# Kernel tuning notes

Hardware: AMD Instinct MI355X
Metric: run time of the kernel (lower is better)

## Reference

```python
import jax, jax.numpy as jnp
import numpy as np

D_MODEL = 1024
HEADS = 16
DK = D_MODEL // HEADS
LAYERS = 4
BATCH = 8
SEQ = 1024
EPS = 1e-5


def _ln2(x):
    # torch LayerNorm([seq_len, d_model]) with default (untrained) affine: gamma=1, beta=0
    m = jnp.mean(x, axis=(1, 2), keepdims=True)
    v = jnp.var(x, axis=(1, 2), keepdims=True)
    return (x - m) * jax.lax.rsqrt(v + EPS)


def _pos_enc(seq_len, d_model):
    pos = jnp.arange(seq_len, dtype=jnp.float32)[:, None]
    i = jnp.arange(d_model)
    angle = pos / jnp.power(1000.0, (2 * (i // 2)).astype(jnp.float32) / d_model)
    return jnp.where(i % 2 == 0, jnp.sin(angle), jnp.cos(angle))  # [S, D]


def setup_inputs() -> dict:
    key = jax.random.key(0)
    ks = jax.random.split(key, 12)
    s = 0.02
    X = jax.random.normal(ks[0], (BATCH, SEQ, D_MODEL), dtype=jnp.float32)
    Wq = jax.random.normal(ks[1], (LAYERS, HEADS, DK, D_MODEL), dtype=jnp.float32) * s
    Wk = jax.random.normal(ks[2], (LAYERS, HEADS, DK, D_MODEL), dtype=jnp.float32) * s
    Wv = jax.random.normal(ks[3], (LAYERS, HEADS, DK, D_MODEL), dtype=jnp.float32) * s
    W0 = jax.random.normal(ks[4], (LAYERS, D_MODEL, D_MODEL), dtype=jnp.float32) * s
    Wr_w = jax.random.normal(ks[5], (LAYERS, D_MODEL, D_MODEL), dtype=jnp.float32) * s
    Wr_b = jax.random.normal(ks[6], (LAYERS, D_MODEL), dtype=jnp.float32) * s
    Wf0_w = jax.random.normal(ks[7], (LAYERS, D_MODEL, D_MODEL), dtype=jnp.float32) * s
    Wf0_b = jax.random.normal(ks[8], (LAYERS, D_MODEL), dtype=jnp.float32) * s
    Wf1_w = jax.random.normal(ks[9], (LAYERS, D_MODEL, D_MODEL), dtype=jnp.float32) * s
    Wf1_b = jax.random.normal(ks[10], (LAYERS, D_MODEL), dtype=jnp.float32) * s
    return {"X": X, "Wq": Wq, "Wk": Wk, "Wv": Wv, "W0": W0,
            "Wr_w": Wr_w, "Wr_b": Wr_b, "Wf0_w": Wf0_w, "Wf0_b": Wf0_b,
            "Wf1_w": Wf1_w, "Wf1_b": Wf1_b}


def reference(X, Wq, Wk, Wv, W0, Wr_w, Wr_b, Wf0_w, Wf0_b, Wf1_w, Wf1_b):
    B, S, D = X.shape
    x = X + _pos_enc(S, D)[None]
    scale = 1.0 / jnp.sqrt(jnp.float32(DK))
    for l in range(LAYERS):
        # batched multi-head projections (equivalent to per-head Linear + concat)
        Q = jnp.einsum('bsd,hkd->bhsk', x, Wq[l])
        K = jnp.einsum('bsd,hkd->bhsk', x, Wk[l])
        V = jnp.einsum('bsd,hkd->bhsk', x, Wv[l])
        scores = jnp.einsum('bhsk,bhtk->bhst', Q, K) * scale
        A = jax.nn.softmax(scores, axis=-1)
        O = jnp.einsum('bhst,bhtk->bhsk', A, V)
        O = O.transpose(0, 2, 1, 3).reshape(B, S, D)  # concat heads on feature dim
        mha = O @ W0[l].T
        r0 = _ln2(x + mha) @ Wr_w[l].T + Wr_b[l]
        ff = jax.nn.relu(r0 @ Wf0_w[l].T + Wf0_b[l]) @ Wf1_w[l].T + Wf1_b[l]
        x = _ln2(ff + r0) @ Wr_w[l].T + Wr_b[l]
    return x
```

## Files before the change

kernel.cpp:

```cpp
#include <hip/hip_runtime.h>
#include <hip/hip_bf16.h>
#include <math.h>

#define D_MODEL 1024
#define HEADS   16
#define DKV     64
#define LAYERS  4
#define BATCH   8
#define SEQ     1024
#define NTOK    (BATCH*SEQ)
#define LN_N    (SEQ*D_MODEL)
#define EPSV    1e-5f

typedef __attribute__((ext_vector_type(8))) short short8;
typedef __attribute__((ext_vector_type(4))) float floatx4;

__device__ __forceinline__ float bf2f(ushort u) {
    union { uint i; float f; } v; v.i = ((uint)u) << 16; return v.f;
}
__device__ __forceinline__ ushort f2bf(float f) {
    union { float f; uint i; } v; v.f = f;
    uint r = (v.i + 0x7fffu + ((v.i >> 16) & 1u)) >> 16;
    return (ushort)r;
}
__device__ __forceinline__ uint cvtpk(float a, float b) {
    uint r;
    asm("v_cvt_pk_bf16_f32 %0, %1, %2" : "=v"(r) : "v"(a), "v"(b));
    return r;
}

__device__ __forceinline__ void gload16(const ushort* g, ushort* l) {
    __builtin_amdgcn_global_load_lds(
        (const __attribute__((address_space(1))) void*)g,
        (__attribute__((address_space(3))) void*)l, 16, 0, 0);
}

__device__ __forceinline__ void gemm_core128(
    const ushort* __restrict__ A, const ushort* __restrict__ B,
    int lda, int ldb, int Kd,
    ushort* ldsA, ushort* ldsB, floatx4 (&acc)[4][4])
{
    const int tid  = threadIdx.x;
    const int lane = tid & 63;
    const int w    = tid >> 6;
    const int wm   = w >> 1, wn = w & 1;
    const int mn   = lane & 15, quad = lane >> 4;
    const int srow = tid >> 2;
    const int scol = (tid & 3) * 8;
    const ushort* ga = A + (size_t)srow * lda + scol;
    const ushort* gb = B + (size_t)srow * ldb + scol;
    ushort* la = ldsA + srow * 32 + scol;
    ushort* lb = ldsB + srow * 32 + scol;

    for (int k0 = 0; k0 < Kd; k0 += 32) {
        gload16(ga + k0, la);
        gload16(ga + (size_t)64 * lda + k0, la + 64 * 32);
        gload16(gb + k0, lb);
        gload16(gb + (size_t)64 * ldb + k0, lb + 64 * 32);
        __syncthreads();
        short8 af[4], bfr[4];
#pragma unroll
        for (int i = 0; i < 4; i++)
            af[i] = *(const short8*)(ldsA + (wm * 64 + i * 16 + mn) * 32 + quad * 8);
#pragma unroll
        for (int j = 0; j < 4; j++)
            bfr[j] = *(const short8*)(ldsB + (wn * 64 + j * 16 + mn) * 32 + quad * 8);
#pragma unroll
        for (int i = 0; i < 4; i++)
#pragma unroll
            for (int j = 0; j < 4; j++)
                acc[i][j] = __builtin_amdgcn_mfma_f32_16x16x32_bf16(af[i], bfr[j], acc[i][j], 0, 0, 0);
        __syncthreads();
    }
}

__global__ __launch_bounds__(256) void gemm_bt128(
    const ushort* __restrict__ A, const ushort* __restrict__ B,
    const float* __restrict__ bias, ushort* __restrict__ C,
    const ushort* __restrict__ resid, float* __restrict__ stats,
    float* __restrict__ outF, int relu)
{
    __shared__ ushort ldsA[128 * 32], ldsB[128 * 32];
    __shared__ float sred1[4], sred2[4];
    floatx4 acc[4][4];
#pragma unroll
    for (int i = 0; i < 4; i++)
#pragma unroll
        for (int j = 0; j < 4; j++) acc[i][j] = (floatx4){0.f, 0.f, 0.f, 0.f};

    gemm_core128(A + (size_t)blockIdx.x * 128 * D_MODEL,
                 B + (size_t)blockIdx.y * 128 * D_MODEL,
                 D_MODEL, D_MODEL, D_MODEL, ldsA, ldsB, acc);

    const int lane = threadIdx.x & 63, w = threadIdx.x >> 6;
    const int wm = w >> 1, wn = w & 1;
    const int mn = lane & 15, quad = lane >> 4;
    float ssum = 0.f, ssq = 0.f;
#pragma unroll
    for (int i = 0; i < 4; i++) {
#pragma unroll
        for (int j = 0; j < 4; j++) {
            int col = blockIdx.y * 128 + wn * 64 + j * 16 + mn;
            float bv = bias ? bias[col] : 0.f;
#pragma unroll
            for (int r = 0; r < 4; r++) {
                int row = blockIdx.x * 128 + wm * 64 + i * 16 + quad * 4 + r;
                float v = acc[i][j][r] + bv;
                if (relu) v = fmaxf(v, 0.f);
                if (resid) {
                    v += bf2f(resid[(size_t)row * D_MODEL + col]);
                    ssum += v; ssq += v * v;
                }
                if (outF) outF[(size_t)row * D_MODEL + col] = v;
                else      C[(size_t)row * D_MODEL + col] = f2bf(v);
            }
        }
    }
    if (stats) {
        for (int o = 1; o < 64; o <<= 1) {
            ssum += __shfl_xor(ssum, o); ssq += __shfl_xor(ssq, o);
        }
        if (lane == 0) { sred1[w] = ssum; sred2[w] = ssq; }
        __syncthreads();
        if (threadIdx.x == 0) {
            int b = blockIdx.x >> 3;
            atomicAdd(&stats[b * 32],      sred1[0] + sred1[1] + sred1[2] + sred1[3]);
            atomicAdd(&stats[b * 32 + 16], sred2[0] + sred2[1] + sred2[2] + sred2[3]);
        }
    }
}

__global__ __launch_bounds__(256) void gemm_qkv(
    const ushort* __restrict__ X, const ushort* __restrict__ Wq,
    const ushort* __restrict__ Wk, const ushort* __restrict__ Wv,
    ushort* __restrict__ Q, ushort* __restrict__ K, ushort* __restrict__ Vt)
{
    __shared__ ushort ldsA[128 * 32], ldsB[128 * 32];
    const int which = blockIdx.y >> 3;
    const int nb = blockIdx.y & 7;
    const ushort* B = (which == 0) ? Wq : (which == 1) ? Wk : Wv;
    floatx4 acc[4][4];
#pragma unroll
    for (int i = 0; i < 4; i++)
#pragma unroll
        for (int j = 0; j < 4; j++) acc[i][j] = (floatx4){0.f, 0.f, 0.f, 0.f};

    gemm_core128(X + (size_t)blockIdx.x * 128 * D_MODEL,
                 B + (size_t)nb * 128 * D_MODEL,
                 D_MODEL, D_MODEL, D_MODEL, ldsA, ldsB, acc);

    const int lane = threadIdx.x & 63, w = threadIdx.x >> 6;
    const int wm = w >> 1, wn = w & 1;
    const int mn = lane & 15, quad = lane >> 4;
    ushort* dst = (which == 0) ? Q : K;
#pragma unroll
    for (int i = 0; i < 4; i++) {
#pragma unroll
        for (int j = 0; j < 4; j++) {
            int col = nb * 128 + wn * 64 + j * 16 + mn;
#pragma unroll
            for (int r = 0; r < 4; r++) {
                int row = blockIdx.x * 128 + wm * 64 + i * 16 + quad * 4 + r;
                ushort v = f2bf(acc[i][j][r]);
                if (which == 2) {
                    int h = col >> 6, kk = col & 63;
                    int b = row >> 10, t = row & 1023;
                    Vt[(((size_t)(b * HEADS + h)) * DKV + kk) * SEQ + t] = v;
                } else {
                    dst[(size_t)row * D_MODEL + col] = v;
                }
            }
        }
    }
}

#define SQK 72
#define SV  136
__global__ __launch_bounds__(256) void flash_attn(
    const ushort* __restrict__ Q, const ushort* __restrict__ K,
    const ushort* __restrict__ Vt, ushort* __restrict__ O)
{
    __shared__ ushort lQ[128 * SQK];
    __shared__ ushort lK[128 * SQK];
    __shared__ ushort lV[64 * SV];
    const int tid = threadIdx.x, lane = tid & 63, w = tid >> 6;
    const int mn = lane & 15, quad = lane >> 4;
    const int pair = blockIdx.x;
    const int qt = blockIdx.y;
    const int b = pair >> 4, h = pair & 15;
    const ushort* Qb = Q + ((size_t)b * SEQ) * D_MODEL + h * DKV;
    const ushort* Kb = K + ((size_t)b * SEQ) * D_MODEL + h * DKV;
    const ushort* Vb = Vt + (size_t)pair * DKV * SEQ;

#pragma unroll
    for (int c = 0; c < 4; c++) {
        int idx = c * 256 + tid;
        int row = idx >> 3, col = (idx & 7) * 8;
        short8 qv = *(const short8*)(Qb + (size_t)(qt * 128 + row) * D_MODEL + col);
        short8 qs;
#pragma unroll
        for (int e = 0; e < 8; e++) qs[e] = (short)f2bf(bf2f((ushort)qv[e]) * 0.125f);
        *(short8*)(lQ + row * SQK + col) = qs;
    }
    short8 kreg[4], vreg[4];
#pragma unroll
    for (int c = 0; c < 4; c++) {
        int idx = c * 256 + tid;
        int row = idx >> 3, col = (idx & 7) * 8;
        kreg[c] = *(const short8*)(Kb + (size_t)row * D_MODEL + col);
        int vr = idx >> 4, vc = (idx & 15) * 8;
        vreg[c] = *(const short8*)(Vb + (size_t)vr * SEQ + vc);
    }
    __syncthreads();

    short8 bq[2][2];
#pragma unroll
    for (int i = 0; i < 2; i++)
#pragma unroll
        for (int kk = 0; kk < 2; kk++)
            bq[i][kk] = *(const short8*)(lQ + (w * 32 + i * 16 + mn) * SQK + kk * 32 + quad * 8);

#pragma unroll
    for (int c = 0; c < 4; c++) {
        int idx = c * 256 + tid;
        int row = idx >> 3, col = (idx & 7) * 8;
        *(short8*)(lK + row * SQK + col) = kreg[c];
        int vr = idx >> 4, vc = (idx & 15) * 8;
        *(short8*)(lV + vr * SV + vc) = vreg[c];
    }
    __syncthreads();

    floatx4 acc_o[2][4];
    float lrow[2] = {0.f, 0.f};
#pragma unroll
    for (int i = 0; i < 2; i++)
#pragma unroll
        for (int jo = 0; jo < 4; jo++) acc_o[i][jo] = (floatx4){0.f, 0.f, 0.f, 0.f};

    for (int tk = 0; tk < 8; tk++) {
        if (tk < 7) {
#pragma unroll
            for (int c = 0; c < 4; c++) {
                int idx = c * 256 + tid;
                int row = idx >> 3, col = (idx & 7) * 8;
                kreg[c] = *(const short8*)(Kb + (size_t)((tk + 1) * 128 + row) * D_MODEL + col);
                int vr = idx >> 4, vc = (idx & 15) * 8;
                vreg[c] = *(const short8*)(Vb + (size_t)vr * SEQ + (tk + 1) * 128 + vc);
            }
        }

        floatx4 s[2][8];
#pragma unroll
        for (int i = 0; i < 2; i++)
#pragma unroll
            for (int j = 0; j < 8; j++) s[i][j] = (floatx4){0.f, 0.f, 0.f, 0.f};
        __builtin_amdgcn_s_setprio(1);
#pragma unroll
        for (int kk = 0; kk < 2; kk++) {
#pragma unroll
            for (int j = 0; j < 8; j++) {
                short8 ak = *(const short8*)(lK + (j * 16 + mn) * SQK + kk * 32 + quad * 8);
                s[0][j] = __builtin_amdgcn_mfma_f32_16x16x32_bf16(ak, bq[0][kk], s[0][j], 0, 0, 0);
                s[1][j] = __builtin_amdgcn_mfma_f32_16x16x32_bf16(ak, bq[1][kk], s[1][j], 0, 0, 0);
            }
        }
        __builtin_amdgcn_s_setprio(0);

#pragma unroll
        for (int i = 0; i < 2; i++) {
            float ps = 0.f;
#pragma unroll
            for (int j = 0; j < 8; j++)
#pragma unroll
                for (int r = 0; r < 4; r++) {
                    float p = __expf(s[i][j][r]);
                    s[i][j][r] = p;
                    ps += p;
                }
            ps += __shfl_xor(ps, 16);
            ps += __shfl_xor(ps, 32);
            lrow[i] += ps;
        }

#pragma unroll
        for (int hf = 0; hf < 2; hf++) {
#pragma unroll
            for (int i = 0; i < 2; i++)
#pragma unroll
                for (int jl = 0; jl < 4; jl++) {
                    int j = hf * 4 + jl;
                    uint2 uu;
                    uu.x = cvtpk(s[i][j][0], s[i][j][1]);
                    uu.y = cvtpk(s[i][j][2], s[i][j][3]);
                    *(uint2*)(lQ + (w * 32 + i * 16 + mn) * SQK + jl * 16 + quad * 4) = uu;
                }
            __builtin_amdgcn_s_setprio(1);
#pragma unroll
            for (int kkl = 0; kkl < 2; kkl++) {
                int kk = hf * 2 + kkl;
                short8 pa0 = *(const short8*)(lQ + (w * 32 + 0  + mn) * SQK + kkl * 32 + quad * 8);
                short8 pa1 = *(const short8*)(lQ + (w * 32 + 16 + mn) * SQK + kkl * 32 + quad * 8);
#pragma unroll
                for (int jo = 0; jo < 4; jo++) {
                    short8 bv = *(const short8*)(lV + (jo * 16 + mn) * SV + kk * 32 + quad * 8);
                    acc_o[0][jo] = __builtin_amdgcn_mfma_f32_16x16x32_bf16(pa0, bv, acc_o[0][jo], 0, 0, 0);
                    acc_o[1][jo] = __builtin_amdgcn_mfma_f32_16x16x32_bf16(pa1, bv, acc_o[1][jo], 0, 0, 0);
                }
            }
            __builtin_amdgcn_s_setprio(0);
        }

        __syncthreads();
        if (tk < 7) {
#pragma unroll
            for (int c = 0; c < 4; c++) {
                int idx = c * 256 + tid;
                int row = idx >> 3, col = (idx & 7) * 8;
                *(short8*)(lK + row * SQK + col) = kreg[c];
                int vr = idx >> 4, vc = (idx & 15) * 8;
                *(short8*)(lV + vr * SV + vc) = vreg[c];
            }
            __syncthreads();
        }
    }

#pragma unroll
    for (int i = 0; i < 2; i++)
#pragma unroll
        for (int r = 0; r < 4; r++) {
            float rs = __shfl(lrow[i], quad * 4 + r);
            float rinv = 1.f / rs;
            int row = qt * 128 + w * 32 + i * 16 + quad * 4 + r;
#pragma unroll
            for (int jo = 0; jo < 4; jo++)
                O[((size_t)b * SEQ + row) * D_MODEL + h * DKV + jo * 16 + mn] =
                    f2bf(acc_o[i][jo][r] * rinv);
        }
}

__global__ __launch_bounds__(256) void cvt_f32_bf16(const float* __restrict__ src,
                                                    ushort* __restrict__ dst) {
    size_t base = ((size_t)blockIdx.x * 256 + threadIdx.x) * 8;
    float4 a = *(const float4*)(src + base);
    float4 b = *(const float4*)(src + base + 4);
    short8 o;
    o[0] = (short)f2bf(a.x); o[1] = (short)f2bf(a.y);
    o[2] = (short)f2bf(a.z); o[3] = (short)f2bf(a.w);
    o[4] = (short)f2bf(b.x); o[5] = (short)f2bf(b.y);
    o[6] = (short)f2bf(b.z); o[7] = (short)f2bf(b.w);
    *(short8*)(dst + base) = o;
}

__global__ __launch_bounds__(256) void add_pos(const float* __restrict__ X,
                                               ushort* __restrict__ x) {
    size_t idx = (size_t)blockIdx.x * 256 + threadIdx.x;
    int d = (int)(idx & (D_MODEL - 1));
    int s = (int)((idx >> 10) & (SEQ - 1));
    float freq = powf(1000.f, (float)(2 * (d >> 1)) * (1.f / (float)D_MODEL));
    float ang = (float)s / freq;
    float pe = (d & 1) ? cosf(ang) : sinf(ang);
    x[idx] = f2bf(X[idx] + pe);
}

__global__ __launch_bounds__(256) void ln_apply(
    const ushort* __restrict__ S, ushort* __restrict__ Y,
    const float* __restrict__ stats)
{
    size_t base = ((size_t)blockIdx.x * 256 + threadIdx.x) * 8;
    int b = blockIdx.x >> 9;
    float mean = stats[b * 32] * (1.f / (float)LN_N);
    float var = stats[b * 32 + 16] * (1.f / (float)LN_N) - mean * mean;
    float r = rsqrtf(var + EPSV);
    short8 sv = *(const short8*)(S + base);
    short8 ov;
#pragma unroll
    for (int i = 0; i < 8; i++) ov[i] = (short)f2bf((bf2f((ushort)sv[i]) - mean) * r);
    *(short8*)(Y + base) = ov;
}

__global__ void zero_stats(float* stats) { stats[threadIdx.x] = 0.f; }

extern "C" void kernel_launch(void* const* d_in, const int* in_sizes, int n_in,
                              void* d_out, int out_size, void* d_ws, size_t ws_size,
                              hipStream_t stream) {
    const float* X    = (const float*)d_in[0];
    const float* Wq   = (const float*)d_in[1];
    const float* Wk   = (const float*)d_in[2];
    const float* Wv   = (const float*)d_in[3];
    const float* W0   = (const float*)d_in[4];
    const float* Wr_w = (const float*)d_in[5];
    const float* Wr_b = (const float*)d_in[6];
    const float* Wf0w = (const float*)d_in[7];
    const float* Wf0b = (const float*)d_in[8];
    const float* Wf1w = (const float*)d_in[9];
    const float* Wf1b = (const float*)d_in[10];
    float* out = (float*)d_out;

    char* ws = (char*)d_ws;
    size_t off = 0;
    auto alloc = [&](size_t bytes) -> void* {
        void* p = ws + off; off += (bytes + 255) & ~(size_t)255; return p;
    };
    const size_t ACT = (size_t)NTOK * D_MODEL * sizeof(ushort);
    const size_t WTE = (size_t)LAYERS * D_MODEL * D_MODEL;
    ushort* x  = (ushort*)alloc(ACT);
    ushort* bQ = (ushort*)alloc(ACT);
    ushort* bK = (ushort*)alloc(ACT);
    ushort* bV = (ushort*)alloc(ACT);
    ushort* bO = (ushort*)alloc(ACT);
    ushort* wq  = (ushort*)alloc(WTE * 2);
    ushort* wk  = (ushort*)alloc(WTE * 2);
    ushort* wv  = (ushort*)alloc(WTE * 2);
    ushort* w0  = (ushort*)alloc(WTE * 2);
    ushort* wr  = (ushort*)alloc(WTE * 2);
    ushort* wf0 = (ushort*)alloc(WTE * 2);
    ushort* wf1 = (ushort*)alloc(WTE * 2);
    float* stats = (float*)alloc(256 * sizeof(float));

    const int EW_BLOCKS = (NTOK * D_MODEL) / (256 * 8);
    const int CVT_BLOCKS = (int)(WTE / (256 * 8));
    const dim3 GEMM_GRID(NTOK / 128, D_MODEL / 128);
    const dim3 QKV_GRID(NTOK / 128, 3 * D_MODEL / 128);
    const dim3 FLASH_GRID(BATCH * HEADS, SEQ / 128);

    cvt_f32_bf16<<<CVT_BLOCKS, 256, 0, stream>>>(Wq,   wq);
    cvt_f32_bf16<<<CVT_BLOCKS, 256, 0, stream>>>(Wk,   wk);
    cvt_f32_bf16<<<CVT_BLOCKS, 256, 0, stream>>>(Wv,   wv);
    cvt_f32_bf16<<<CVT_BLOCKS, 256, 0, stream>>>(W0,   w0);
    cvt_f32_bf16<<<CVT_BLOCKS, 256, 0, stream>>>(Wr_w, wr);
    cvt_f32_bf16<<<CVT_BLOCKS, 256, 0, stream>>>(Wf0w, wf0);
    cvt_f32_bf16<<<CVT_BLOCKS, 256, 0, stream>>>(Wf1w, wf1);

    add_pos<<<(NTOK * D_MODEL) / 256, 256, 0, stream>>>(X, x);

    for (int l = 0; l < LAYERS; l++) {
        const size_t WO = (size_t)l * D_MODEL * D_MODEL;
        const ushort* Wq_l  = wq  + WO;
        const ushort* Wk_l  = wk  + WO;
        const ushort* Wv_l  = wv  + WO;
        const ushort* W0_l  = w0  + WO;
        const ushort* Wr_l  = wr  + WO;
        const ushort* W0w_l = wf0 + WO;
        const ushort* W1w_l = wf1 + WO;
        const float* Wrb_l = Wr_b + (size_t)l * D_MODEL;
        const float* W0b_l = Wf0b + (size_t)l * D_MODEL;
        const float* W1b_l = Wf1b + (size_t)l * D_MODEL;

        gemm_qkv<<<QKV_GRID, 256, 0, stream>>>(x, Wq_l, Wk_l, Wv_l, bQ, bK, bV);

        flash_attn<<<FLASH_GRID, 256, 0, stream>>>(bQ, bK, bV, bO);

        zero_stats<<<1, 256, 0, stream>>>(stats);
        gemm_bt128<<<GEMM_GRID, 256, 0, stream>>>(bO, W0_l, nullptr, bK,
            x, stats, nullptr, 0);
        ln_apply<<<EW_BLOCKS, 256, 0, stream>>>(bK, bO, stats);
        gemm_bt128<<<GEMM_GRID, 256, 0, stream>>>(bO, Wr_l, Wrb_l, bV,
            nullptr, nullptr, nullptr, 0);
        gemm_bt128<<<GEMM_GRID, 256, 0, stream>>>(bV, W0w_l, W0b_l, bQ,
            nullptr, nullptr, nullptr, 1);
        zero_stats<<<1, 256, 0, stream>>>(stats);
        gemm_bt128<<<GEMM_GRID, 256, 0, stream>>>(bQ, W1w_l, W1b_l, bK,
            bV, stats, nullptr, 0);
        ln_apply<<<EW_BLOCKS, 256, 0, stream>>>(bK, bO, stats);
        gemm_bt128<<<GEMM_GRID, 256, 0, stream>>>(bO, Wr_l, Wrb_l, x,
            nullptr, nullptr, (l == LAYERS - 1) ? out : nullptr, 0);
    }
}
```

Before: 1.627 ms.

## Double-buffer GEMM LDS tiles, remap blocks per XCD, vectorize V-transpose stores

The shared GEMM core now double-buffers the A/B tiles in LDS. It prefetches the next K-slice with global_load_lds while the MFMAs run on the current slice, which removes one barrier per iteration. Both GEMM kernels remap the linear block id so that blocks on the same XCD share A row-panels, aiming for better L2 reuse. The V-transpose epilogue packs four consecutive tokens into one 8-byte store instead of scalar 2-byte writes. In exchange, LDS use per block doubles, which may reduce occupancy.

New measurement: 1.629 ms. No clear change (+0.2%).

```diff
diff --git a/kernel.cpp b/kernel.cpp
--- a/kernel.cpp
+++ b/kernel.cpp
@@ -35,6 +35,7 @@
         (__attribute__((address_space(3))) void*)l, 16, 0, 0);
 }
 
+#define TBUF (128*32)
 __device__ __forceinline__ void gemm_core128(
     const ushort* __restrict__ A, const ushort* __restrict__ B,
     int lda, int ldb, int Kd,
@@ -52,25 +53,37 @@
     ushort* la = ldsA + srow * 32 + scol;
     ushort* lb = ldsB + srow * 32 + scol;
 
+    gload16(ga, la);
+    gload16(ga + (size_t)64 * lda, la + 64 * 32);
+    gload16(gb, lb);
+    gload16(gb + (size_t)64 * ldb, lb + 64 * 32);
+    __syncthreads();
+
+    int cur = 0;
     for (int k0 = 0; k0 < Kd; k0 += 32) {
-        gload16(ga + k0, la);
-        gload16(ga + (size_t)64 * lda + k0, la + 64 * 32);
-        gload16(gb + k0, lb);
-        gload16(gb + (size_t)64 * ldb + k0, lb + 64 * 32);
-        __syncthreads();
+        const int nxt = cur ^ 1;
+        if (k0 + 32 < Kd) {
+            gload16(ga + k0 + 32, la + nxt * TBUF);
+            gload16(ga + (size_t)64 * lda + k0 + 32, la + nxt * TBUF + 64 * 32);
+            gload16(gb + k0 + 32, lb + nxt * TBUF);
+            gload16(gb + (size_t)64 * ldb + k0 + 32, lb + nxt * TBUF + 64 * 32);
+        }
+        const ushort* cA = ldsA + cur * TBUF;
+        const ushort* cB = ldsB + cur * TBUF;
         short8 af[4], bfr[4];
 #pragma unroll
         for (int i = 0; i < 4; i++)
-            af[i] = *(const short8*)(ldsA + (wm * 64 + i * 16 + mn) * 32 + quad * 8);
+            af[i] = *(const short8*)(cA + (wm * 64 + i * 16 + mn) * 32 + quad * 8);
 #pragma unroll
         for (int j = 0; j < 4; j++)
-            bfr[j] = *(const short8*)(ldsB + (wn * 64 + j * 16 + mn) * 32 + quad * 8);
+            bfr[j] = *(const short8*)(cB + (wn * 64 + j * 16 + mn) * 32 + quad * 8);
 #pragma unroll
         for (int i = 0; i < 4; i++)
 #pragma unroll
             for (int j = 0; j < 4; j++)
                 acc[i][j] = __builtin_amdgcn_mfma_f32_16x16x32_bf16(af[i], bfr[j], acc[i][j], 0, 0, 0);
         __syncthreads();
+        cur = nxt;
     }
 }
 
@@ -80,16 +93,20 @@
     const ushort* __restrict__ resid, float* __restrict__ stats,
     float* __restrict__ outF, int relu)
 {
-    __shared__ ushort ldsA[128 * 32], ldsB[128 * 32];
+    __shared__ ushort ldsA[2 * TBUF], ldsB[2 * TBUF];
     __shared__ float sred1[4], sred2[4];
+    const int lid = blockIdx.y * 64 + blockIdx.x;
+    const int xcd = lid & 7, idx = lid >> 3;
+    const int bx = xcd * 8 + (idx >> 3);
+    const int by = idx & 7;
     floatx4 acc[4][4];
 #pragma unroll
     for (int i = 0; i < 4; i++)
 #pragma unroll
         for (int j = 0; j < 4; j++) acc[i][j] = (floatx4){0.f, 0.f, 0.f, 0.f};
 
-    gemm_core128(A + (size_t)blockIdx.x * 128 * D_MODEL,
-                 B + (size_t)blockIdx.y * 128 * D_MODEL,
+    gemm_core128(A + (size_t)bx * 128 * D_MODEL,
+                 B + (size_t)by * 128 * D_MODEL,
                  D_MODEL, D_MODEL, D_MODEL, ldsA, ldsB, acc);
 
     const int lane = threadIdx.x & 63, w = threadIdx.x >> 6;
@@ -100,11 +117,11 @@
     for (int i = 0; i < 4; i++) {
 #pragma unroll
         for (int j = 0; j < 4; j++) {
-            int col = blockIdx.y * 128 + wn * 64 + j * 16 + mn;
+            int col = by * 128 + wn * 64 + j * 16 + mn;
             float bv = bias ? bias[col] : 0.f;
 #pragma unroll
             for (int r = 0; r < 4; r++) {
-                int row = blockIdx.x * 128 + wm * 64 + i * 16 + quad * 4 + r;
+                int row = bx * 128 + wm * 64 + i * 16 + quad * 4 + r;
                 float v = acc[i][j][r] + bv;
                 if (relu) v = fmaxf(v, 0.f);
                 if (resid) {
@@ -123,7 +140,7 @@
         if (lane == 0) { sred1[w] = ssum; sred2[w] = ssq; }
         __syncthreads();
         if (threadIdx.x == 0) {
-            int b = blockIdx.x >> 3;
+            int b = bx >> 3;
             atomicAdd(&stats[b * 32],      sred1[0] + sred1[1] + sred1[2] + sred1[3]);
             atomicAdd(&stats[b * 32 + 16], sred2[0] + sred2[1] + sred2[2] + sred2[3]);
         }
@@ -135,9 +152,13 @@
     const ushort* __restrict__ Wk, const ushort* __restrict__ Wv,
     ushort* __restrict__ Q, ushort* __restrict__ K, ushort* __restrict__ Vt)
 {
-    __shared__ ushort ldsA[128 * 32], ldsB[128 * 32];
-    const int which = blockIdx.y >> 3;
-    const int nb = blockIdx.y & 7;
+    __shared__ ushort ldsA[2 * TBUF], ldsB[2 * TBUF];
+    const int lid = blockIdx.y * 64 + blockIdx.x;
+    const int xcd = lid & 7, idx = lid >> 3;
+    const int bx = xcd * 8 + idx / 24;
+    const int byy = idx % 24;
+    const int which = byy >> 3;
+    const int nb = byy & 7;
     const ushort* B = (which == 0) ? Wq : (which == 1) ? Wk : Wv;
     floatx4 acc[4][4];
 #pragma unroll
@@ -145,29 +166,39 @@
 #pragma unroll
         for (int j = 0; j < 4; j++) acc[i][j] = (floatx4){0.f, 0.f, 0.f, 0.f};
 
-    gemm_core128(X + (size_t)blockIdx.x * 128 * D_MODEL,
+    gemm_core128(X + (size_t)bx * 128 * D_MODEL,
                  B + (size_t)nb * 128 * D_MODEL,
                  D_MODEL, D_MODEL, D_MODEL, ldsA, ldsB, acc);
 
     const int lane = threadIdx.x & 63, w = threadIdx.x >> 6;
     const int wm = w >> 1, wn = w & 1;
     const int mn = lane & 15, quad = lane >> 4;
-    ushort* dst = (which == 0) ? Q : K;
-#pragma unroll
-    for (int i = 0; i < 4; i++) {
-#pragma unroll
-        for (int j = 0; j < 4; j++) {
-            int col = nb * 128 + wn * 64 + j * 16 + mn;
-#pragma unroll
-            for (int r = 0; r < 4; r++) {
-                int row = blockIdx.x * 128 + wm * 64 + i * 16 + quad * 4 + r;
-                ushort v = f2bf(acc[i][j][r]);
-                if (which == 2) {
-                    int h = col >> 6, kk = col & 63;
-                    int b = row >> 10, t = row & 1023;
-                    Vt[(((size_t)(b * HEADS + h)) * DKV + kk) * SEQ + t] = v;
-                } else {
-                    dst[(size_t)row * D_MODEL + col] = v;
+    if (which == 2) {
+#pragma unroll
+        for (int i = 0; i < 4; i++) {
+#pragma unroll
+            for (int j = 0; j < 4; j++) {
+                int col = nb * 128 + wn * 64 + j * 16 + mn;
+                int h = col >> 6, kk = col & 63;
+                int row0 = bx * 128 + wm * 64 + i * 16 + quad * 4;
+                int b = row0 >> 10, t0 = row0 & 1023;
+                uint2 uu;
+                uu.x = cvtpk(acc[i][j][0], acc[i][j][1]);
+                uu.y = cvtpk(acc[i][j][2], acc[i][j][3]);
+                *(uint2*)(Vt + (((size_t)(b * HEADS + h)) * DKV + kk) * SEQ + t0) = uu;
+            }
+        }
+    } else {
+        ushort* dst = (which == 0) ? Q : K;
+#pragma unroll
+        for (int i = 0; i < 4; i++) {
+#pragma unroll
+            for (int j = 0; j < 4; j++) {
+                int col = nb * 128 + wn * 64 + j * 16 + mn;
+#pragma unroll
+                for (int r = 0; r < 4; r++) {
+                    int row = bx * 128 + wm * 64 + i * 16 + quad * 4 + r;
+                    dst[(size_t)row * D_MODEL + col] = f2bf(acc[i][j][r]);
                 }
             }
         }
```
